# Kernel optimization log

Hardware: AMD Instinct MI355X
Metric: run time of the kernel (lower is better)

## Reference

```python
import jax, jax.numpy as jnp
import numpy as np

N = 100000
E = 2000000
LN_EPS = 1e-5


def _ln(x, g, b):
    m = jnp.mean(x, axis=-1, keepdims=True)
    v = jnp.mean((x - m) ** 2, axis=-1, keepdims=True)
    return (x - m) * jax.lax.rsqrt(v + LN_EPS) * g + b


def _gcn_conv(x, W, b, row, col, n_nodes):
    xw = x @ W  # [N, out_dim]
    deg = jax.ops.segment_sum(jnp.ones((row.shape[0],), xw.dtype), row, num_segments=n_nodes) + 1.0
    dinv = jax.lax.rsqrt(deg)
    norm = dinv[row] * dinv[col]  # [E]
    msg = xw[col] * norm[:, None]  # gather + scale, [E, out_dim]
    agg = jax.ops.segment_sum(msg, row, num_segments=n_nodes)
    self_loop = xw * (dinv * dinv)[:, None]
    return agg + self_loop + b


def setup_inputs() -> dict:
    key = jax.random.key(0)
    ks = jax.random.split(key, 32)
    s = 0.05
    d = dict(
        coords=jax.random.normal(ks[0], (N, 2), jnp.float32),
        features=jax.random.normal(ks[1], (N, 3), jnp.float32),
        edge_index=jax.random.randint(ks[2], (2, E), 0, N, jnp.int32),
        # spatial encoder FFN: 2->128, two hidden 128->128 (relu+LN), last 128->128 (relu)
        fw0=jax.random.normal(ks[3], (2, 128), jnp.float32) * s,
        fb0=jnp.zeros((128,), jnp.float32),
        fg0=jnp.ones((128,), jnp.float32),
        fe0=jnp.zeros((128,), jnp.float32),
        fw1=jax.random.normal(ks[4], (128, 128), jnp.float32) * s,
        fb1=jnp.zeros((128,), jnp.float32),
        fg1=jnp.ones((128,), jnp.float32),
        fe1=jnp.zeros((128,), jnp.float32),
        fw2=jax.random.normal(ks[5], (128, 128), jnp.float32) * s,
        fb2=jnp.zeros((128,), jnp.float32),
        fg2=jnp.ones((128,), jnp.float32),
        fe2=jnp.zeros((128,), jnp.float32),
        fw3=jax.random.normal(ks[6], (128, 128), jnp.float32) * s,
        fb3=jnp.zeros((128,), jnp.float32),
        # dec: 128->64->32->16 with tanh between
        dw0=jax.random.normal(ks[7], (128, 64), jnp.float32) * s,
        db0=jnp.zeros((64,), jnp.float32),
        dw1=jax.random.normal(ks[8], (64, 32), jnp.float32) * s,
        db1=jnp.zeros((32,), jnp.float32),
        dw2=jax.random.normal(ks[9], (32, 16), jnp.float32) * s,
        db2=jnp.zeros((16,), jnp.float32),
        # GCN convs: (3+16)->64, 64->64; fc 64->1
        cw1=jax.random.normal(ks[10], (19, 64), jnp.float32) * s,
        cb1=jnp.zeros((64,), jnp.float32),
        cw2=jax.random.normal(ks[11], (64, 64), jnp.float32) * s,
        cb2=jnp.zeros((64,), jnp.float32),
        ow=jax.random.normal(ks[12], (64, 1), jnp.float32) * s,
        ob=jnp.zeros((1,), jnp.float32),
    )
    return d


def reference(coords, features, edge_index,
              fw0, fb0, fg0, fe0, fw1, fb1, fg1, fe1, fw2, fb2, fg2, fe2, fw3, fb3,
              dw0, db0, dw1, db1, dw2, db2,
              cw1, cb1, cw2, cb2, ow, ob):
    # positional encoder FFN (dropout disabled / eval mode)
    h = _ln(jax.nn.relu(coords @ fw0 + fb0), fg0, fe0)
    h = _ln(jax.nn.relu(h @ fw1 + fb1), fg1, fe1)
    h = _ln(jax.nn.relu(h @ fw2 + fb2), fg2, fe2)
    h = jax.nn.relu(h @ fw3 + fb3)
    # decoder to emb_dim
    emb = jnp.tanh(h @ dw0 + db0)
    emb = jnp.tanh(emb @ dw1 + db1)
    emb = emb @ dw2 + db2  # [N, 16]
    x = jnp.concatenate([features, emb], axis=-1)  # [N, 19]
    row, col = edge_index[0], edge_index[1]
    h1 = jax.nn.relu(_gcn_conv(x, cw1, cb1, row, col, x.shape[0]))
    h2 = _gcn_conv(h1, cw2, cb2, row, col, x.shape[0])
    out = h2 @ ow + ob  # [N, 1]
    return out
```

## Files before the change

### kernel.cpp

```cpp
#include <hip/hip_runtime.h>
#include <hip/hip_bf16.h>
#include <math.h>

#define TM 64
#define XROW 64
#define NSEG 8

typedef float v2f __attribute__((ext_vector_type(2)));
typedef float f32x4 __attribute__((ext_vector_type(4)));
typedef __bf16 bf16x8 __attribute__((ext_vector_type(8)));
typedef unsigned short u16x8 __attribute__((ext_vector_type(8)));
typedef unsigned int uint_t;
typedef unsigned short ushort_t;

__device__ __forceinline__ v2f fma2(v2f a, v2f b, v2f c) {
    return __builtin_elementwise_fma(a, b, c);
}
__device__ __forceinline__ v2f splat2(float s) { return (v2f){s, s}; }
__device__ __forceinline__ v2f max02(v2f a) {
    return (v2f){fmaxf(a.x, 0.0f), fmaxf(a.y, 0.0f)};
}
__device__ __forceinline__ uint_t pack_bf16(float lo, float hi) {
    uint_t r;
    asm volatile("v_cvt_pk_bf16_f32 %0, %1, %2" : "=v"(r) : "v"(lo), "v"(hi));
    return r;
}
__device__ __forceinline__ float bf16_f(ushort_t u) {
    union { uint_t i; float f; } c; c.i = ((uint_t)u) << 16; return c.f;
}
__device__ __forceinline__ float blo(uint_t u) {
    union { uint_t i; float f; } c; c.i = u << 16; return c.f;
}
__device__ __forceinline__ float bhi(uint_t u) {
    union { uint_t i; float f; } c; c.i = u & 0xffff0000u; return c.f;
}

__device__ __forceinline__ int aaddr(int node, int feat) {
    return (node * 256 + feat * 2) ^ ((node & 15) << 4);
}

__global__ void prepw_kernel(const float* __restrict__ W, ushort_t* __restrict__ out,
                             int K, int N) {
    int idx = blockIdx.x * 256 + threadIdx.x;
    int total = 2 * K * N;
    if (idx >= total) return;
    int j    = idx & 7;
    int lane = (idx >> 3) & 63;
    int rest = idx >> 9;
    int ncb  = N >> 4;
    int cb   = rest % ncb;
    int r2   = rest / ncb;
    int nkk  = K >> 5;
    int kk   = r2 % nkk;
    int h    = r2 / nkk;
    int k = kk * 32 + (lane >> 4) * 8 + j;
    int n = cb * 16 + (lane & 15);
    float wv = W[k * N + n];
    ushort_t hi = (ushort_t)pack_bf16(wv, wv);
    if (h == 0) {
        out[idx] = hi;
    } else {
        float res = wv - bf16_f(hi);
        out[idx] = (ushort_t)pack_bf16(res, res);
    }
}

__global__ __launch_bounds__(256, 4) void ffn_kernel(
    const float* __restrict__ coords, const float* __restrict__ features,
    const float* __restrict__ dinv,
    const float* __restrict__ fw0, const float* __restrict__ fb0,
    const float* __restrict__ fg0, const float* __restrict__ fe0,
    const ushort_t* __restrict__ wswz,
    const float* __restrict__ fb1, const float* __restrict__ fg1, const float* __restrict__ fe1,
    const float* __restrict__ fb2, const float* __restrict__ fg2, const float* __restrict__ fe2,
    const float* __restrict__ fb3,
    const float* __restrict__ dw0, const float* __restrict__ db0,
    const float* __restrict__ dw1, const float* __restrict__ db1,
    const float* __restrict__ dw2, const float* __restrict__ db2,
    char* __restrict__ xsb, int n_nodes)
{
    __shared__ __align__(16) char abuf[16384];
    __shared__ ushort_t tbuf[128][64];
    __shared__ float ps1[4][64];
    __shared__ float ps2[4][64];

    const int t    = threadIdx.x;
    const int lane = t & 63;
    const int w    = __builtin_amdgcn_readfirstlane(t >> 6);
    const int jw   = w * 32;
    const int n0   = blockIdx.x * TM;

    int g = n0 + lane;
    if (g >= n_nodes) g = n_nodes - 1;

    {
        v2f acc[16];
        float2 c = *(const float2*)&coords[(size_t)g * 2];
        v2f cx = splat2(c.x), cy = splat2(c.y);
        #pragma unroll
        for (int q = 0; q < 16; q++) {
            int j = jw + 2 * q;
            v2f w0 = *(const v2f*)&fw0[j];
            v2f w1 = *(const v2f*)&fw0[128 + j];
            v2f bb = *(const v2f*)&fb0[j];
            acc[q] = max02(fma2(cx, w0, fma2(cy, w1, bb)));
        }
        float s1 = 0.f, s2 = 0.f;
        #pragma unroll
        for (int q = 0; q < 16; q++) {
            s1 += acc[q].x + acc[q].y;
            s2 += acc[q].x * acc[q].x + acc[q].y * acc[q].y;
        }
        ps1[w][lane] = s1; ps2[w][lane] = s2;
        __syncthreads();
        float t1 = ps1[0][lane] + ps1[1][lane] + ps1[2][lane] + ps1[3][lane];
        float t2 = ps2[0][lane] + ps2[1][lane] + ps2[2][lane] + ps2[3][lane];
        float mean = t1 * (1.0f / 128.0f);
        float var  = t2 * (1.0f / 128.0f) - mean * mean;
        float inv  = rsqrtf(var + 1e-5f);
        v2f mean2 = splat2(mean), inv2 = splat2(inv);
        #pragma unroll
        for (int q = 0; q < 16; q++) {
            int j = jw + 2 * q;
            v2f gm = *(const v2f*)&fg0[j];
            v2f bt = *(const v2f*)&fe0[j];
            v2f o = fma2((acc[q] - mean2) * inv2, gm, bt);
            *(uint_t*)(abuf + aaddr(lane, j)) = pack_bf16(o.x, o.y);
        }
        __syncthreads();
    }

    auto mfma_layer = [&](const ushort_t* Wb, const float* __restrict__ bias) {
        f32x4 acc[2][4] = {};
        #pragma unroll
        for (int kk = 0; kk < 4; kk++) {
            bf16x8 B[2][2];
            #pragma unroll
            for (int cb2 = 0; cb2 < 2; cb2++) {
                int cb = 2 * w + cb2;
                #pragma unroll
                for (int h = 0; h < 2; h++) {
                    const ushort_t* p = Wb + (size_t)(((h * 4 + kk) * 8 + cb) * 64 + lane) * 8;
                    B[cb2][h] = *(const bf16x8*)p;
                }
            }
            #pragma unroll
            for (int rb = 0; rb < 4; rb++) {
                int node = rb * 16 + (lane & 15);
                bf16x8 A = *(const bf16x8*)(abuf + aaddr(node, kk * 32 + (lane >> 4) * 8));
                #pragma unroll
                for (int cb2 = 0; cb2 < 2; cb2++) {
                    acc[cb2][rb] = __builtin_amdgcn_mfma_f32_16x16x32_bf16(A, B[cb2][0], acc[cb2][rb], 0, 0, 0);
                    acc[cb2][rb] = __builtin_amdgcn_mfma_f32_16x16x32_bf16(A, B[cb2][1], acc[cb2][rb], 0, 0, 0);
                }
            }
        }
        __syncthreads();
        float bv0 = bias[jw + (lane & 15)];
        float bv1 = bias[jw + 16 + (lane & 15)];
        #pragma unroll
        for (int cb2 = 0; cb2 < 2; cb2++) {
            int col = jw + cb2 * 16 + (lane & 15);
            float bv = cb2 ? bv1 : bv0;
            #pragma unroll
            for (int rb = 0; rb < 4; rb++) {
                #pragma unroll
                for (int r = 0; r < 4; r++) {
                    float v = fmaxf(acc[cb2][rb][r] + bv, 0.0f);
                    int node = rb * 16 + (lane >> 4) * 4 + r;
                    *(ushort_t*)(abuf + aaddr(node, col)) = (ushort_t)pack_bf16(v, v);
                }
            }
        }
        __syncthreads();
    };

    auto ln_pass = [&](const float* __restrict__ gam, const float* __restrict__ bet) {
        int node = t >> 2;
        int part = t & 3;
        float vals[32];
        float s1 = 0.f, s2 = 0.f;
        #pragma unroll
        for (int q = 0; q < 4; q++) {
            int f0 = part * 32 + q * 8;
            u16x8 u = *(const u16x8*)(abuf + aaddr(node, f0));
            #pragma unroll
            for (int i = 0; i < 8; i++) {
                float v = bf16_f(u[i]);
                vals[q * 8 + i] = v;
                s1 += v; s2 += v * v;
            }
        }
        s1 += __shfl_xor(s1, 1); s1 += __shfl_xor(s1, 2);
        s2 += __shfl_xor(s2, 1); s2 += __shfl_xor(s2, 2);
        float mean = s1 * (1.0f / 128.0f);
        float var  = s2 * (1.0f / 128.0f) - mean * mean;
        float inv  = rsqrtf(var + 1e-5f);
        #pragma unroll
        for (int q = 0; q < 4; q++) {
            int f0 = part * 32 + q * 8;
            uint_t ov[4];
            #pragma unroll
            for (int p = 0; p < 4; p++) {
                v2f gm = *(const v2f*)&gam[f0 + 2 * p];
                v2f bt = *(const v2f*)&bet[f0 + 2 * p];
                float a = (vals[q * 8 + 2 * p]     - mean) * inv * gm.x + bt.x;
                float b = (vals[q * 8 + 2 * p + 1] - mean) * inv * gm.y + bt.y;
                ov[p] = pack_bf16(a, b);
            }
            uint4 uv = make_uint4(ov[0], ov[1], ov[2], ov[3]);
            *(uint4*)(abuf + aaddr(node, f0)) = uv;
        }
        __syncthreads();
    };

    mfma_layer(wswz,         fb1); ln_pass(fg1, fe1);
    mfma_layer(wswz + 32768, fb2); ln_pass(fg2, fe2);
    mfma_layer(wswz + 65536, fb3);

    {
        #pragma unroll
        for (int q = 0; q < 4; q++) {
            int f0 = jw + q * 8;
            u16x8 u = *(const u16x8*)(abuf + aaddr(lane, f0));
            #pragma unroll
            for (int i = 0; i < 8; i++) tbuf[f0 + i][lane] = u[i];
        }
        __syncthreads();
    }

    {
        const int j16 = w * 16;
        v2f d0[8];
        #pragma unroll
        for (int q = 0; q < 8; q++) d0[q] = *(const v2f*)&db0[j16 + 2 * q];
        #pragma unroll 4
        for (int k = 0; k < 128; k++) {
            v2f av = splat2(bf16_f(tbuf[k][lane]));
            const v2f* W2 = (const v2f*)(dw0 + k * 64 + j16);
            #pragma unroll
            for (int q = 0; q < 8; q++) d0[q] = fma2(av, W2[q], d0[q]);
        }
        #pragma unroll
        for (int q = 0; q < 8; q++) d0[q] = (v2f){tanhf(d0[q].x), tanhf(d0[q].y)};
        __syncthreads();
        #pragma unroll
        for (int q = 0; q < 8; q++) {
            uint_t r = pack_bf16(d0[q].x, d0[q].y);
            tbuf[j16 + 2 * q][lane]     = (ushort_t)r;
            tbuf[j16 + 2 * q + 1][lane] = (ushort_t)(r >> 16);
        }
        __syncthreads();
    }

    {
        const int j8 = w * 8;
        v2f d1[4];
        #pragma unroll
        for (int q = 0; q < 4; q++) d1[q] = *(const v2f*)&db1[j8 + 2 * q];
        #pragma unroll 4
        for (int k = 0; k < 64; k++) {
            v2f av = splat2(bf16_f(tbuf[k][lane]));
            const v2f* W2 = (const v2f*)(dw1 + k * 32 + j8);
            #pragma unroll
            for (int q = 0; q < 4; q++) d1[q] = fma2(av, W2[q], d1[q]);
        }
        #pragma unroll
        for (int q = 0; q < 4; q++) d1[q] = (v2f){tanhf(d1[q].x), tanhf(d1[q].y)};
        __syncthreads();
        #pragma unroll
        for (int q = 0; q < 4; q++) {
            uint_t r = pack_bf16(d1[q].x, d1[q].y);
            tbuf[j8 + 2 * q][lane]     = (ushort_t)r;
            tbuf[j8 + 2 * q + 1][lane] = (ushort_t)(r >> 16);
        }
        __syncthreads();
    }

    {
        const int j4 = w * 4;
        v2f d2[2];
        #pragma unroll
        for (int q = 0; q < 2; q++) d2[q] = *(const v2f*)&db2[j4 + 2 * q];
        #pragma unroll 4
        for (int k = 0; k < 32; k++) {
            v2f av = splat2(bf16_f(tbuf[k][lane]));
            const v2f* W2 = (const v2f*)(dw2 + k * 16 + j4);
            d2[0] = fma2(av, W2[0], d2[0]);
            d2[1] = fma2(av, W2[1], d2[1]);
        }
        __syncthreads();
        #pragma unroll
        for (int q = 0; q < 2; q++) {
            uint_t r = pack_bf16(d2[q].x, d2[q].y);
            tbuf[j4 + 2 * q][lane]     = (ushort_t)r;
            tbuf[j4 + 2 * q + 1][lane] = (ushort_t)(r >> 16);
        }
        __syncthreads();
    }

    {
        const int nn = t & 63;
        const int jg = t >> 6;
        int gg = n0 + nn;
        if (gg < n_nodes && jg < 3) {
            float dgg = dinv[gg];
            char* rp = xsb + (size_t)gg * XROW;
            if (jg == 0) {
                float4 f;
                f.x = features[(size_t)gg * 3 + 0] * dgg;
                f.y = features[(size_t)gg * 3 + 1] * dgg;
                f.z = features[(size_t)gg * 3 + 2] * dgg;
                f.w = 0.0f;
                *(float4*)rp = f;
            } else {
                int e0 = (jg - 1) * 8;
                uint_t u[4];
                #pragma unroll
                for (int p = 0; p < 4; p++) {
                    float lo = bf16_f(tbuf[e0 + 2 * p][nn]) * dgg;
                    float hi = bf16_f(tbuf[e0 + 2 * p + 1][nn]) * dgg;
                    u[p] = pack_bf16(lo, hi);
                }
                uint4 uv = make_uint4(u[0], u[1], u[2], u[3]);
                *(uint4*)(rp + 16 + (jg - 1) * 16) = uv;
            }
        }
    }
}

__global__ void deg8_kernel(const int* __restrict__ row, int* __restrict__ cnt8,
                            int E_, int Nn) {
    int s = blockIdx.x & (NSEG - 1);
    int* cs = cnt8 + (size_t)s * Nn;
    int e4 = (blockIdx.x * blockDim.x + threadIdx.x) * 4;
    if (e4 + 3 < E_) {
        int4 r = *(const int4*)&row[e4];
        atomicAdd(&cs[r.x], 1); atomicAdd(&cs[r.y], 1);
        atomicAdd(&cs[r.z], 1); atomicAdd(&cs[r.w], 1);
    } else {
        for (int e = e4; e < E_; e++) atomicAdd(&cs[row[e]], 1);
    }
}

__global__ void scan1_kernel(const int* __restrict__ in, int* __restrict__ out,
                             int* __restrict__ bsum, int n) {
    __shared__ int tmp[256];
    int t = threadIdx.x, b = blockIdx.x;
    int base = b * 2048 + t * 8;
    int v[8]; int s = 0;
    #pragma unroll
    for (int q = 0; q < 8; q++) {
        int idx = base + q;
        v[q] = (idx < n) ? in[idx] : 0;
        s += v[q];
    }
    tmp[t] = s; __syncthreads();
    #pragma unroll
    for (int d = 1; d < 256; d <<= 1) {
        int add = (t >= d) ? tmp[t - d] : 0;
        __syncthreads();
        tmp[t] += add;
        __syncthreads();
    }
    int run = tmp[t] - s;
    #pragma unroll
    for (int q = 0; q < 8; q++) {
        int idx = base + q;
        if (idx < n) out[idx] = run;
        run += v[q];
    }
    if (t == 255) bsum[b] = tmp[t];
}

__global__ void scan2_kernel(int* __restrict__ bsum, int B) {
    __shared__ int tmp[512];
    int t = threadIdx.x;
    tmp[t] = (t < B) ? bsum[t] : 0; __syncthreads();
    #pragma unroll
    for (int d = 1; d < 512; d <<= 1) {
        int add = (t >= d) ? tmp[t - d] : 0;
        __syncthreads();
        tmp[t] += add;
        __syncthreads();
    }
    if (t < B) bsum[t] = tmp[t];
}

__global__ void scanfix_kernel(int* __restrict__ data, const int* __restrict__ bsum, int n) {
    int i = blockIdx.x * 256 + threadIdx.x;
    if (i >= n) return;
    int b = i >> 11;
    if (b > 0) data[i] += bsum[b - 1];
}

__global__ void dinv_kernel(const int* __restrict__ cnt8, float* __restrict__ dinv, int Nn) {
    int i = blockIdx.x * 256 + threadIdx.x;
    if (i >= Nn) return;
    int s = 0;
    #pragma unroll
    for (int q = 0; q < NSEG; q++) s += cnt8[(size_t)q * Nn + i];
    dinv[i] = rsqrtf((float)s + 1.0f);
}

__global__ void scatter_kernel(const int* __restrict__ row, const int* __restrict__ col,
                               int* __restrict__ fill8, int* __restrict__ es,
                               int E_, int Nn) {
    int s = blockIdx.x & (NSEG - 1);
    int* fs = fill8 + (size_t)s * Nn;
    int e4 = (blockIdx.x * blockDim.x + threadIdx.x) * 4;
    if (e4 + 3 < E_) {
        int4 r = *(const int4*)&row[e4];
        int4 c = *(const int4*)&col[e4];
        es[atomicAdd(&fs[r.x], 1)] = c.x;
        es[atomicAdd(&fs[r.y], 1)] = c.y;
        es[atomicAdd(&fs[r.z], 1)] = c.z;
        es[atomicAdd(&fs[r.w], 1)] = c.w;
    } else {
        for (int e = e4; e < E_; e++) {
            int p = atomicAdd(&fs[row[e]], 1);
            es[p] = col[e];
        }
    }
}

__global__ void prep_kernel(const float* __restrict__ cw2, const float* __restrict__ cb2,
                            const float* __restrict__ ow, const float* __restrict__ ob,
                            float* __restrict__ wb) {
    int i = threadIdx.x;
    if (i < 64) {
        float a = 0.f;
        for (int j = 0; j < 64; j++) a += cw2[i * 64 + j] * ow[j];
        wb[i] = a;
    }
    if (i == 0) {
        float bb = 0.f;
        for (int j = 0; j < 64; j++) bb += cb2[j] * ow[j];
        wb[64] = bb + ob[0];
    }
}

__global__ __launch_bounds__(256) void node1g_kernel(
    const int* __restrict__ fill8, const int* __restrict__ cnt8, const int* __restrict__ es,
    const float* __restrict__ dinv, const char* __restrict__ xsb,
    const float* __restrict__ cw1, const float* __restrict__ cb1,
    const float* __restrict__ wb, float* __restrict__ ss, int n)
{
    __shared__ float w[19 * 64];
    __shared__ float bbs[64];
    __shared__ float wes[64];
    for (int i = threadIdx.x; i < 19 * 64; i += 256) w[i] = cw1[i];
    for (int i = threadIdx.x; i < 64; i += 256) { bbs[i] = cb1[i]; wes[i] = wb[i]; }
    __syncthreads();
    const int t  = threadIdx.x;
    const int oc = t & 7;
    const int i  = blockIdx.x * 32 + (t >> 3);
    if (i >= n) return;
    const float di = dinv[i];

    float af[19];
    #pragma unroll
    for (int q = 0; q < 19; q++) af[q] = 0.f;

    auto addrow = [&](const char* rp) {
        float4 F = *(const float4*)rp;
        uint4 U0 = *(const uint4*)(rp + 16);
        uint4 U1 = *(const uint4*)(rp + 32);
        af[0] += F.x; af[1] += F.y; af[2] += F.z;
        af[3]  += blo(U0.x); af[4]  += bhi(U0.x);
        af[5]  += blo(U0.y); af[6]  += bhi(U0.y);
        af[7]  += blo(U0.z); af[8]  += bhi(U0.z);
        af[9]  += blo(U0.w); af[10] += bhi(U0.w);
        af[11] += blo(U1.x); af[12] += bhi(U1.x);
        af[13] += blo(U1.y); af[14] += bhi(U1.y);
        af[15] += blo(U1.z); af[16] += bhi(U1.z);
        af[17] += blo(U1.w); af[18] += bhi(U1.w);
    };

    if (oc == 0) addrow(xsb + (size_t)i * XROW);
    const int end = fill8[(size_t)oc * n + i];
    const int dgs = cnt8[(size_t)oc * n + i];
    for (int e = end - dgs; e < end; e++) {
        int c = es[e];
        addrow(xsb + (size_t)c * XROW);
    }

    float a19[19];
    #pragma unroll
    for (int q = 0; q < 19; q++) {
        float v = af[q];
        v += __shfl_xor(v, 1);
        v += __shfl_xor(v, 2);
        v += __shfl_xor(v, 4);
        a19[q] = v * di;
    }

    const int j0 = oc * 8;
    v2f am[4];
    const v2f* w2  = (const v2f*)w;
    const v2f* bb2 = (const v2f*)bbs;
    #pragma unroll
    for (int q = 0; q < 4; q++) am[q] = bb2[j0 / 2 + q];
    #pragma unroll
    for (int k = 0; k < 19; k++) {
        v2f v = splat2(a19[k]);
        #pragma unroll
        for (int q = 0; q < 4; q++) am[q] = fma2(v, w2[k * 32 + j0 / 2 + q], am[q]);
    }
    const v2f* we2 = (const v2f*)wes;
    v2f sv2 = {0.f, 0.f};
    #pragma unroll
    for (int q = 0; q < 4; q++) sv2 = fma2(max02(am[q]), we2[j0 / 2 + q], sv2);
    float sv = sv2.x + sv2.y;
    sv += __shfl_xor(sv, 1);
    sv += __shfl_xor(sv, 2);
    sv += __shfl_xor(sv, 4);
    if (oc == 0) ss[i] = di * sv;
}

__global__ __launch_bounds__(256) void outg_kernel(
    const int* __restrict__ fill8, const int* __restrict__ cnt8, const int* __restrict__ es,
    const float* __restrict__ dinv, const float* __restrict__ ss,
    const float* __restrict__ wb, float* __restrict__ out, int n)
{
    const int t  = threadIdx.x;
    const int oc = t & 7;
    const int i  = blockIdx.x * 32 + (t >> 3);
    if (i >= n) return;
    const int end = fill8[(size_t)oc * n + i];
    const int dgs = cnt8[(size_t)oc * n + i];
    float sum = (oc == 0) ? ss[i] : 0.f;
    for (int e = end - dgs; e < end; e++) {
        int c = es[e];
        sum += ss[c];
    }
    sum += __shfl_xor(sum, 1);
    sum += __shfl_xor(sum, 2);
    sum += __shfl_xor(sum, 4);
    if (oc == 0) out[i] = wb[64] + dinv[i] * sum;
}

extern "C" void kernel_launch(void* const* d_in, const int* in_sizes, int n_in,
                              void* d_out, int out_size, void* d_ws, size_t ws_size,
                              hipStream_t stream) {
    const float* coords   = (const float*)d_in[0];
    const float* features = (const float*)d_in[1];
    const int*   eidx     = (const int*)d_in[2];
    const float* fw0 = (const float*)d_in[3];
    const float* fb0 = (const float*)d_in[4];
    const float* fg0 = (const float*)d_in[5];
    const float* fe0 = (const float*)d_in[6];
    const float* fw1 = (const float*)d_in[7];
    const float* fb1 = (const float*)d_in[8];
    const float* fg1 = (const float*)d_in[9];
    const float* fe1 = (const float*)d_in[10];
    const float* fw2 = (const float*)d_in[11];
    const float* fb2 = (const float*)d_in[12];
    const float* fg2 = (const float*)d_in[13];
    const float* fe2 = (const float*)d_in[14];
    const float* fw3 = (const float*)d_in[15];
    const float* fb3 = (const float*)d_in[16];
    const float* dw0 = (const float*)d_in[17];
    const float* db0 = (const float*)d_in[18];
    const float* dw1 = (const float*)d_in[19];
    const float* db1 = (const float*)d_in[20];
    const float* dw2 = (const float*)d_in[21];
    const float* db2 = (const float*)d_in[22];
    const float* cw1 = (const float*)d_in[23];
    const float* cb1 = (const float*)d_in[24];
    const float* cw2 = (const float*)d_in[25];
    const float* cb2 = (const float*)d_in[26];
    const float* ow  = (const float*)d_in[27];
    const float* ob  = (const float*)d_in[28];
    float* out = (float*)d_out;

    const int Nn = in_sizes[0] / 2;
    const int E_ = in_sizes[2] / 2;
    const int n8 = NSEG * Nn;
    const int NBS = (n8 + 2047) / 2048;
    const int NO = (Nn * 8 + 255) / 256;
    const int NT = (Nn + TM - 1) / TM;
    const int NE = (E_ / 4 + 255) / 256;

    char* ws = (char*)d_ws;
    size_t o = 0;
    char*  xsb   = (char*) (ws + o); o += (size_t)Nn * XROW;
    int*   cnt8  = (int*)  (ws + o); o += (size_t)n8 * sizeof(int);
    int*   fill8 = (int*)  (ws + o); o += (size_t)n8 * sizeof(int);
    int*   bsum  = (int*)  (ws + o); o += 512 * sizeof(int);
    float* dinv  = (float*)(ws + o); o += (size_t)Nn * sizeof(float);
    float* ssb   = (float*)(ws + o); o += (size_t)Nn * sizeof(float);
    int*   es    = (int*)  (ws + o); o += (size_t)E_ * sizeof(int);
    float* wb    = (float*)(ws + o); o += 80 * sizeof(float);
    o = (o + 15) & ~(size_t)15;
    ushort_t* wswz = (ushort_t*)(ws + o); o += 3 * 32768 * sizeof(ushort_t);

    hipMemsetAsync(cnt8, 0, (size_t)n8 * sizeof(int), stream);

    prepw_kernel<<<(32768 + 255) / 256, 256, 0, stream>>>(fw1, wswz,         128, 128);
    prepw_kernel<<<(32768 + 255) / 256, 256, 0, stream>>>(fw2, wswz + 32768, 128, 128);
    prepw_kernel<<<(32768 + 255) / 256, 256, 0, stream>>>(fw3, wswz + 65536, 128, 128);

    deg8_kernel<<<NE, 256, 0, stream>>>(eidx, cnt8, E_, Nn);
    scan1_kernel<<<NBS, 256, 0, stream>>>(cnt8, fill8, bsum, n8);
    scan2_kernel<<<1, 512, 0, stream>>>(bsum, NBS);
    scanfix_kernel<<<(n8 + 255) / 256, 256, 0, stream>>>(fill8, bsum, n8);
    dinv_kernel<<<(Nn + 255) / 256, 256, 0, stream>>>(cnt8, dinv, Nn);
    scatter_kernel<<<NE, 256, 0, stream>>>(eidx, eidx + E_, fill8, es, E_, Nn);

    ffn_kernel<<<NT, 256, 0, stream>>>(
        coords, features, dinv,
        fw0, fb0, fg0, fe0,
        wswz,
        fb1, fg1, fe1, fb2, fg2, fe2, fb3,
        dw0, db0, dw1, db1, dw2, db2, xsb, Nn);

    prep_kernel<<<1, 64, 0, stream>>>(cw2, cb2, ow, ob, wb);
    node1g_kernel<<<NO, 256, 0, stream>>>(fill8, cnt8, es, dinv, xsb, cw1, cb1, wb, ssb, Nn);
    outg_kernel<<<NO, 256, 0, stream>>>(fill8, cnt8, es, dinv, ssb, wb, out, Nn);
}
```

Measured before the change: 374.2 us.

## Move first decoder layer to bf16 MFMA and raise FFN occupancy

Replaces the scalar FMA loop for the 128->64 decoder layer with bf16 MFMA over the shared activation buffer, using weights pre-swizzled by an extra prepw launch (hi/lo split). This halves the transpose buffer and raises launch bounds to 6 waves per SIMD to improve occupancy. It also zero-fills the unused tail of each xsb row. The goal is less VALU work in the FFN kernel, at the cost of tighter register limits that could cause spills.

```diff
diff --git a/kernel.cpp b/kernel.cpp
--- a/kernel.cpp
+++ b/kernel.cpp
@@ -65,7 +65,7 @@
     }
 }
 
-__global__ __launch_bounds__(256, 4) void ffn_kernel(
+__global__ __launch_bounds__(256, 6) void ffn_kernel(
     const float* __restrict__ coords, const float* __restrict__ features,
     const float* __restrict__ dinv,
     const float* __restrict__ fw0, const float* __restrict__ fb0,
@@ -74,13 +74,13 @@
     const float* __restrict__ fb1, const float* __restrict__ fg1, const float* __restrict__ fe1,
     const float* __restrict__ fb2, const float* __restrict__ fg2, const float* __restrict__ fe2,
     const float* __restrict__ fb3,
-    const float* __restrict__ dw0, const float* __restrict__ db0,
+    const float* __restrict__ db0,
     const float* __restrict__ dw1, const float* __restrict__ db1,
     const float* __restrict__ dw2, const float* __restrict__ db2,
     char* __restrict__ xsb, int n_nodes)
 {
     __shared__ __align__(16) char abuf[16384];
-    __shared__ ushort_t tbuf[128][64];
+    __shared__ ushort_t tbuf[64][64];
     __shared__ float ps1[4][64];
     __shared__ float ps2[4][64];
 
@@ -175,6 +175,37 @@
         __syncthreads();
     };
 
+    auto mfma_d0 = [&](const ushort_t* Wb, const float* __restrict__ bias) {
+        f32x4 acc[4] = {};
+        #pragma unroll
+        for (int kk = 0; kk < 4; kk++) {
+            const ushort_t* p0 = Wb + (size_t)(((0 * 4 + kk) * 4 + w) * 64 + lane) * 8;
+            const ushort_t* p1 = Wb + (size_t)(((1 * 4 + kk) * 4 + w) * 64 + lane) * 8;
+            bf16x8 B0 = *(const bf16x8*)p0;
+            bf16x8 B1 = *(const bf16x8*)p1;
+            #pragma unroll
+            for (int rb = 0; rb < 4; rb++) {
+                int node = rb * 16 + (lane & 15);
+                bf16x8 A = *(const bf16x8*)(abuf + aaddr(node, kk * 32 + (lane >> 4) * 8));
+                acc[rb] = __builtin_amdgcn_mfma_f32_16x16x32_bf16(A, B0, acc[rb], 0, 0, 0);
+                acc[rb] = __builtin_amdgcn_mfma_f32_16x16x32_bf16(A, B1, acc[rb], 0, 0, 0);
+            }
+        }
+        __syncthreads();
+        int col = w * 16 + (lane & 15);
+        float bv = bias[col];
+        #pragma unroll
+        for (int rb = 0; rb < 4; rb++) {
+            #pragma unroll
+            for (int r = 0; r < 4; r++) {
+                float v = tanhf(acc[rb][r] + bv);
+                int node = rb * 16 + (lane >> 4) * 4 + r;
+                *(ushort_t*)(abuf + aaddr(node, col)) = (ushort_t)pack_bf16(v, v);
+            }
+        }
+        __syncthreads();
+    };
+
     auto ln_pass = [&](const float* __restrict__ gam, const float* __restrict__ bet) {
         int node = t >> 2;
         int part = t & 3;
@@ -217,38 +248,15 @@
     mfma_layer(wswz,         fb1); ln_pass(fg1, fe1);
     mfma_layer(wswz + 32768, fb2); ln_pass(fg2, fe2);
     mfma_layer(wswz + 65536, fb3);
+    mfma_d0(wswz + 98304, db0);
 
     {
         #pragma unroll
-        for (int q = 0; q < 4; q++) {
-            int f0 = jw + q * 8;
+        for (int q = 0; q < 2; q++) {
+            int f0 = w * 16 + q * 8;
             u16x8 u = *(const u16x8*)(abuf + aaddr(lane, f0));
             #pragma unroll
             for (int i = 0; i < 8; i++) tbuf[f0 + i][lane] = u[i];
-        }
-        __syncthreads();
-    }
-
-    {
-        const int j16 = w * 16;
-        v2f d0[8];
-        #pragma unroll
-        for (int q = 0; q < 8; q++) d0[q] = *(const v2f*)&db0[j16 + 2 * q];
-        #pragma unroll 4
-        for (int k = 0; k < 128; k++) {
-            v2f av = splat2(bf16_f(tbuf[k][lane]));
-            const v2f* W2 = (const v2f*)(dw0 + k * 64 + j16);
-            #pragma unroll
-            for (int q = 0; q < 8; q++) d0[q] = fma2(av, W2[q], d0[q]);
-        }
-        #pragma unroll
-        for (int q = 0; q < 8; q++) d0[q] = (v2f){tanhf(d0[q].x), tanhf(d0[q].y)};
-        __syncthreads();
-        #pragma unroll
-        for (int q = 0; q < 8; q++) {
-            uint_t r = pack_bf16(d0[q].x, d0[q].y);
-            tbuf[j16 + 2 * q][lane]     = (ushort_t)r;
-            tbuf[j16 + 2 * q + 1][lane] = (ushort_t)(r >> 16);
         }
         __syncthreads();
     }
@@ -303,7 +311,7 @@
         const int nn = t & 63;
         const int jg = t >> 6;
         int gg = n0 + nn;
-        if (gg < n_nodes && jg < 3) {
+        if (gg < n_nodes) {
             float dgg = dinv[gg];
             char* rp = xsb + (size_t)gg * XROW;
             if (jg == 0) {
@@ -313,7 +321,7 @@
                 f.z = features[(size_t)gg * 3 + 2] * dgg;
                 f.w = 0.0f;
                 *(float4*)rp = f;
-            } else {
+            } else if (jg < 3) {
                 int e0 = (jg - 1) * 8;
                 uint_t u[4];
                 #pragma unroll
@@ -324,6 +332,8 @@
                 }
                 uint4 uv = make_uint4(u[0], u[1], u[2], u[3]);
                 *(uint4*)(rp + 16 + (jg - 1) * 16) = uv;
+            } else {
+                *(uint4*)(rp + 48) = make_uint4(0, 0, 0, 0);
             }
         }
     }
@@ -593,13 +603,14 @@
     int*   es    = (int*)  (ws + o); o += (size_t)E_ * sizeof(int);
     float* wb    = (float*)(ws + o); o += 80 * sizeof(float);
     o = (o + 15) & ~(size_t)15;
-    ushort_t* wswz = (ushort_t*)(ws + o); o += 3 * 32768 * sizeof(ushort_t);
+    ushort_t* wswz = (ushort_t*)(ws + o); o += (3 * 32768 + 16384) * sizeof(ushort_t);
 
     hipMemsetAsync(cnt8, 0, (size_t)n8 * sizeof(int), stream);
 
     prepw_kernel<<<(32768 + 255) / 256, 256, 0, stream>>>(fw1, wswz,         128, 128);
     prepw_kernel<<<(32768 + 255) / 256, 256, 0, stream>>>(fw2, wswz + 32768, 128, 128);
     prepw_kernel<<<(32768 + 255) / 256, 256, 0, stream>>>(fw3, wswz + 65536, 128, 128);
+    prepw_kernel<<<(16384 + 255) / 256, 256, 0, stream>>>(dw0, wswz + 98304, 128, 64);
 
     deg8_kernel<<<NE, 256, 0, stream>>>(eidx, cnt8, E_, Nn);
     scan1_kernel<<<NBS, 256, 0, stream>>>(cnt8, fill8, bsum, n8);
@@ -613,7 +624,8 @@
         fw0, fb0, fg0, fe0,
         wswz,
         fb1, fg1, fe1, fb2, fg2, fe2, fb3,
-        dw0, db0, dw1, db1, dw2, db2, xsb, Nn);
+        db0,
+        dw1, db1, dw2, db2, xsb, Nn);
 
     prep_kernel<<<1, 64, 0, stream>>>(cw2, cb2, ow, ob, wb);
     node1g_kernel<<<NO, 256, 0, stream>>>(fill8, cnt8, es, dinv, xsb, cw1, cb1, wb, ssb, Nn);
```

After: 412.3 us. 10.2% more time.
